# Kernel optimization log

Measured on AMD Instinct MI355X. Metric: run time of the kernel, lower is better.

## Reference

```python
import jax, jax.numpy as jnp
import numpy as np

B, T, N, D, K, H = 32, 24, 2048, 64, 32, 16  # batch, timesteps, nodes, dim_in=dim_out, embed_dim, HT_Tem


def setup_inputs() -> dict:
    key = jax.random.key(0)
    ks = jax.random.split(key, 6)
    return {
        "eb": jax.random.normal(ks[0], (B, T, N, D), dtype=jnp.float32),
        "node_embeddings": jax.random.normal(ks[1], (N, K), dtype=jnp.float32),
        "time_eb": jax.random.normal(ks[2], (B, T, K), dtype=jnp.float32),
        "adj": jax.random.normal(ks[3], (K, H, T), dtype=jnp.float32),
        "weights_pool": jax.random.normal(ks[4], (K, D, D), dtype=jnp.float32),
        "bias_pool": jax.random.normal(ks[5], (K, D), dtype=jnp.float32),
    }


def reference(eb, node_embeddings, time_eb, adj, weights_pool, bias_pool):
    # adj_dynamics: [H, T, N] (torch computes nht then permutes to htn)
    adj_dyn = jnp.einsum('nk,kht->htn', node_embeddings, adj)
    # hypergraph aggregation: [B, H, N, D]
    hyper = jnp.einsum('htn,btnd->bhnd', adj_dyn, eb)
    # de-aggregation back to time axis: [B, T, N, D]
    ret = jnp.einsum('htn,bhnd->btnd', adj_dyn, hyper)
    # per-(b,t) generated weights [B, T, D, D] and bias [B, T, 1, D]
    weights = jnp.einsum('btd,dio->btio', time_eb, weights_pool)
    bias = jnp.einsum('btd,do->bto', time_eb, bias_pool)[:, :, None, :]
    out = jnp.einsum('btni,btio->btno', ret, weights) + bias
    return jax.nn.leaky_relu(out + eb, negative_slope=0.01)
```

## Files before the change

### kernel.cpp

```cpp
#include <hip/hip_runtime.h>

#define B_ 32
#define T_ 24
#define N_ 2048
#define D_ 64
#define K_ 32
#define H_ 16
#define NB 16

typedef __attribute__((ext_vector_type(8))) short bf16x8;
typedef __attribute__((ext_vector_type(4))) float f32x4;

__device__ __forceinline__ unsigned short f2bf(float f) {
    unsigned int u = __float_as_uint(f);
    return (unsigned short)((u + 0x7FFFu + ((u >> 16) & 1u)) >> 16);
}
__device__ __forceinline__ float bf2f(unsigned short h) {
    return __uint_as_float(((unsigned int)h) << 16);
}

__global__ void k_prepM(const float* __restrict__ ne, const float* __restrict__ adj,
                        unsigned short* __restrict__ M2) {
    __shared__ float s_ne[K_];
    __shared__ float s_ad[H_ * T_];
    const int n = blockIdx.x;
    const int tid = threadIdx.x;
    if (tid < K_) s_ne[tid] = ne[n * K_ + tid];
    __syncthreads();
    for (int f = tid; f < H_ * T_; f += 64) {
        const int h = f / T_, t = f % T_;
        float a = 0.f;
#pragma unroll
        for (int k = 0; k < K_; ++k) a += s_ne[k] * adj[(k * H_ + h) * T_ + t];
        s_ad[f] = a;
    }
    __syncthreads();
    unsigned short* dst = M2 + (size_t)(n >> 4) * (T_ * T_ * 16) + (n & 15) * T_;
    for (int m = tid; m < T_ * T_; m += 64) {
        const int t = m / T_, t2 = m % T_;
        float a = 0.f;
#pragma unroll
        for (int h = 0; h < H_; ++h) a += s_ad[h * T_ + t] * s_ad[h * T_ + t2];
        dst[t * (16 * T_) + t2] = f2bf(a);
    }
}

__global__ __launch_bounds__(256) void k_prepW(const float* __restrict__ te,
                                               const float* __restrict__ wp,
                                               const float* __restrict__ bp,
                                               unsigned short* __restrict__ Wt,
                                               float* __restrict__ bias) {
    const int bt = blockIdx.x;
    const int tid = threadIdx.x;
    __shared__ float s_te[K_];
    __shared__ float s_W[D_ * D_];
    if (tid < K_) s_te[tid] = te[bt * K_ + tid];
    __syncthreads();
    float4 acc[4] = {};
    for (int k = 0; k < K_; ++k) {
        const float tk = s_te[k];
        const float4* row = (const float4*)(wp + (size_t)k * (D_ * D_));
#pragma unroll
        for (int i = 0; i < 4; ++i) {
            float4 v = row[tid + i * 256];
            acc[i].x += tk * v.x; acc[i].y += tk * v.y;
            acc[i].z += tk * v.z; acc[i].w += tk * v.w;
        }
    }
    float4* sW4 = (float4*)s_W;
#pragma unroll
    for (int i = 0; i < 4; ++i) sW4[tid + i * 256] = acc[i];
    if (tid < D_) {
        float a = 0.f;
#pragma unroll
        for (int k = 0; k < K_; ++k) a += s_te[k] * bp[k * D_ + tid];
        bias[bt * D_ + tid] = a;
    }
    __syncthreads();
    const int o = tid >> 2;
    const int i0 = (tid & 3) * 16;
    unsigned short* dst = Wt + (size_t)bt * (D_ * D_) + o * D_ + i0;
#pragma unroll
    for (int j = 0; j < 16; j += 4) {
        ushort4 u;
        u.x = f2bf(s_W[(i0 + j + 0) * D_ + o]);
        u.y = f2bf(s_W[(i0 + j + 1) * D_ + o]);
        u.z = f2bf(s_W[(i0 + j + 2) * D_ + o]);
        u.w = f2bf(s_W[(i0 + j + 3) * D_ + o]);
        *(ushort4*)(dst + j) = u;
    }
}

__global__ __launch_bounds__(512, 2) void k_fused(const float* __restrict__ eb,
                                                  const unsigned short* __restrict__ M2,
                                                  const unsigned short* __restrict__ Wt,
                                                  const float* __restrict__ bias,
                                                  float* __restrict__ out) {
    const int b = blockIdx.y;
    const int nb = blockIdx.x * NB;
    const int tid = threadIdx.x;
    const int wave = tid >> 6, lane = tid & 63;
    const int lr = lane & 15, lh = lane >> 4;

    __shared__ unsigned short s_eb[T_ * NB * D_];
    __shared__ unsigned short s_M[T_ * NB * T_];

    {
        const float* ebb = eb + (size_t)(b * T_) * N_ * D_;
#pragma unroll
        for (int it = 0; it < 12; ++it) {
            const int f4 = it * 512 + tid;
            const int t = f4 >> 8;
            const int n = (f4 >> 4) & 15;
            const int d0 = (f4 & 15) * 4;
            const float4 v = *(const float4*)(ebb + ((size_t)t * N_ + nb + n) * D_ + d0);
            ushort4 u;
            u.x = f2bf(v.x); u.y = f2bf(v.y); u.z = f2bf(v.z); u.w = f2bf(v.w);
            const int inrow = (d0 * 2) ^ ((n & 7) << 4);
            *(ushort4*)((char*)s_eb + t * (NB * 128) + n * 128 + inrow) = u;
        }
    }
    {
        const unsigned short* Mblk = M2 + (size_t)blockIdx.x * (T_ * T_ * 16);
#pragma unroll
        for (int it = 0; it < 18; ++it) {
            const int e = it * 512 + tid;
            s_M[e] = Mblk[e];
        }
    }
    __syncthreads();

    const char* ebase = (const char*)s_eb;
    const int sw = (lr & 7) << 4;
    const int tb = wave * 3;

    const unsigned short* mrow = s_M + tb * (16 * T_) + lr * T_;
    const char* base0 = ebase + lr * 128 + ((lh * 16) ^ sw);
    const char* base1 = ebase + lr * 128 + ((((lh + 4) * 16)) ^ sw);

    float acc[3][16];
#pragma unroll
    for (int tt = 0; tt < 3; ++tt)
#pragma unroll
        for (int j = 0; j < 16; ++j) acc[tt][j] = 0.f;

#pragma unroll
    for (int tp = 0; tp < T_; ++tp) {
        const float m0 = bf2f(mrow[tp]);
        const float m1 = bf2f(mrow[384 + tp]);
        const float m2 = bf2f(mrow[768 + tp]);
        const bf16x8 e0 = *(const bf16x8*)(base0 + tp * 2048);
        const bf16x8 e1 = *(const bf16x8*)(base1 + tp * 2048);
#pragma unroll
        for (int q = 0; q < 8; ++q) {
            const float ea = bf2f((unsigned short)e0[q]);
            const float eb2 = bf2f((unsigned short)e1[q]);
            acc[0][q] += m0 * ea; acc[0][8 + q] += m0 * eb2;
            acc[1][q] += m1 * ea; acc[1][8 + q] += m1 * eb2;
            acc[2][q] += m2 * ea; acc[2][8 + q] += m2 * eb2;
        }
    }

    bf16x8 Af[3][2];
#pragma unroll
    for (int tt = 0; tt < 3; ++tt)
#pragma unroll
        for (int j = 0; j < 8; ++j) {
            Af[tt][0][j] = (short)f2bf(acc[tt][j]);
            Af[tt][1][j] = (short)f2bf(acc[tt][8 + j]);
        }

#pragma unroll
    for (int tt = 0; tt < 3; ++tt) {
        const int t = tb + tt;
        const int bt = b * T_ + t;
        const unsigned short* Wb = Wt + (size_t)bt * (D_ * D_);
        f32x4 C[4] = {};
#pragma unroll
        for (int ot = 0; ot < 4; ++ot) {
            const bf16x8 B0 = *(const bf16x8*)(Wb + (ot * 16 + lr) * D_ + lh * 8);
            const bf16x8 B1 = *(const bf16x8*)(Wb + (ot * 16 + lr) * D_ + 32 + lh * 8);
            C[ot] = __builtin_amdgcn_mfma_f32_16x16x32_bf16(Af[tt][0], B0, C[ot], 0, 0, 0);
            C[ot] = __builtin_amdgcn_mfma_f32_16x16x32_bf16(Af[tt][1], B1, C[ot], 0, 0, 0);
        }
        float bv[4];
#pragma unroll
        for (int ot = 0; ot < 4; ++ot) bv[ot] = bias[bt * D_ + ot * 16 + lr];

        float* obt = out + ((size_t)bt * N_ + nb) * D_;
#pragma unroll
        for (int r = 0; r < 4; ++r) {
            const int nn = lh * 4 + r;
            const char* erow = ebase + (t * NB + nn) * 128;
            const int swn = (nn & 7) << 4;
#pragma unroll
            for (int ot = 0; ot < 4; ++ot) {
                const int o = ot * 16 + lr;
                const unsigned short eu =
                    *(const unsigned short*)(erow + ((o * 2) ^ swn));
                float v = C[ot][r] + bv[ot] + bf2f(eu);
                v = v >= 0.f ? v : 0.01f * v;
                obt[(size_t)nn * D_ + o] = v;
            }
        }
    }
}

extern "C" void kernel_launch(void* const* d_in, const int* in_sizes, int n_in,
                              void* d_out, int out_size, void* d_ws, size_t ws_size,
                              hipStream_t stream) {
    const float* eb  = (const float*)d_in[0];
    const float* ne  = (const float*)d_in[1];
    const float* te  = (const float*)d_in[2];
    const float* adj = (const float*)d_in[3];
    const float* wp  = (const float*)d_in[4];
    const float* bp  = (const float*)d_in[5];
    float* out = (float*)d_out;

    char* ws = (char*)d_ws;
    const size_t M_bytes  = (size_t)N_ * T_ * T_ * 2;
    const size_t Wt_bytes = (size_t)B_ * T_ * D_ * D_ * 2;
    unsigned short* M2 = (unsigned short*)ws;
    unsigned short* Wt = (unsigned short*)(ws + M_bytes);
    float* bias        = (float*)(ws + M_bytes + Wt_bytes);

    k_prepM<<<N_, 64, 0, stream>>>(ne, adj, M2);
    k_prepW<<<B_ * T_, 256, 0, stream>>>(te, wp, bp, Wt, bias);
    k_fused<<<dim3(N_ / NB, B_), 512, 0, stream>>>(eb, M2, Wt, bias, out);
}
```

Baseline: 284.6 us.

## Shrink node tile to 8, remap lanes, build MFMA A-fragments via ds_bpermute

Halves the node block to 8 with 256-thread blocks, each wave running two passes over timesteps. Each lane now accumulates 8 d-values for one node, and the MFMA A operand is assembled from those lanes with ds_bpermute. The bias and residual are preloaded into the MFMA accumulator, and the shared-memory swizzle is redone for the new layout. The aim is a smaller LDS footprint and more resident blocks; the cost is half-empty MFMA rows (only 8 of 16 used), duplicated W loads per block, and extra permute instructions.

```diff
diff --git a/kernel.cpp b/kernel.cpp
--- a/kernel.cpp
+++ b/kernel.cpp
@@ -6,10 +6,11 @@
 #define D_ 64
 #define K_ 32
 #define H_ 16
-#define NB 16
+#define NB 8
 
 typedef __attribute__((ext_vector_type(8))) short bf16x8;
 typedef __attribute__((ext_vector_type(4))) float f32x4;
+typedef __attribute__((ext_vector_type(4))) int i32x4;
 
 __device__ __forceinline__ unsigned short f2bf(float f) {
     unsigned int u = __float_as_uint(f);
@@ -35,13 +36,13 @@
         s_ad[f] = a;
     }
     __syncthreads();
-    unsigned short* dst = M2 + (size_t)(n >> 4) * (T_ * T_ * 16) + (n & 15) * T_;
+    unsigned short* dst = M2 + (size_t)(n >> 3) * (T_ * T_ * NB) + (n & 7) * T_;
     for (int m = tid; m < T_ * T_; m += 64) {
         const int t = m / T_, t2 = m % T_;
         float a = 0.f;
 #pragma unroll
         for (int h = 0; h < H_; ++h) a += s_ad[h * T_ + t] * s_ad[h * T_ + t2];
-        dst[t * (16 * T_) + t2] = f2bf(a);
+        dst[t * (NB * T_) + t2] = f2bf(a);
     }
 }
 
@@ -91,7 +92,7 @@
     }
 }
 
-__global__ __launch_bounds__(512, 2) void k_fused(const float* __restrict__ eb,
+__global__ __launch_bounds__(256, 4) void k_fused(const float* __restrict__ eb,
                                                   const unsigned short* __restrict__ M2,
                                                   const unsigned short* __restrict__ Wt,
                                                   const float* __restrict__ bias,
@@ -101,106 +102,123 @@
     const int tid = threadIdx.x;
     const int wave = tid >> 6, lane = tid & 63;
     const int lr = lane & 15, lh = lane >> 4;
+    const int ln = lane & 7;
+    const int dh = lane >> 3;
 
     __shared__ unsigned short s_eb[T_ * NB * D_];
     __shared__ unsigned short s_M[T_ * NB * T_];
 
     {
-        const float* ebb = eb + (size_t)(b * T_) * N_ * D_;
 #pragma unroll
         for (int it = 0; it < 12; ++it) {
-            const int f4 = it * 512 + tid;
-            const int t = f4 >> 8;
-            const int n = (f4 >> 4) & 15;
-            const int d0 = (f4 & 15) * 4;
-            const float4 v = *(const float4*)(ebb + ((size_t)t * N_ + nb + n) * D_ + d0);
+            const int f4 = it * 256 + tid;
+            const int t = f4 >> 7;
+            const int rem = f4 & 127;
+            const int n = rem >> 4;
+            const int d0 = (rem & 15) * 4;
+            const float4 v = *(const float4*)(eb + ((size_t)(b * T_ + t) * N_ + nb + n) * D_ + d0);
             ushort4 u;
             u.x = f2bf(v.x); u.y = f2bf(v.y); u.z = f2bf(v.z); u.w = f2bf(v.w);
-            const int inrow = (d0 * 2) ^ ((n & 7) << 4);
-            *(ushort4*)((char*)s_eb + t * (NB * 128) + n * 128 + inrow) = u;
+            const int dh0 = d0 >> 3;
+            const int slot = dh0 * 8 + (n ^ dh0);
+            *(ushort4*)((char*)s_eb + t * 1024 + slot * 16 + (d0 & 7) * 2) = u;
         }
     }
     {
-        const unsigned short* Mblk = M2 + (size_t)blockIdx.x * (T_ * T_ * 16);
-#pragma unroll
-        for (int it = 0; it < 18; ++it) {
-            const int e = it * 512 + tid;
-            s_M[e] = Mblk[e];
-        }
-    }
-    __syncthreads();
-
-    const char* ebase = (const char*)s_eb;
-    const int sw = (lr & 7) << 4;
-    const int tb = wave * 3;
-
-    const unsigned short* mrow = s_M + tb * (16 * T_) + lr * T_;
-    const char* base0 = ebase + lr * 128 + ((lh * 16) ^ sw);
-    const char* base1 = ebase + lr * 128 + ((((lh + 4) * 16)) ^ sw);
-
-    float acc[3][16];
-#pragma unroll
-    for (int tt = 0; tt < 3; ++tt)
-#pragma unroll
-        for (int j = 0; j < 16; ++j) acc[tt][j] = 0.f;
-
-#pragma unroll
-    for (int tp = 0; tp < T_; ++tp) {
-        const float m0 = bf2f(mrow[tp]);
-        const float m1 = bf2f(mrow[384 + tp]);
-        const float m2 = bf2f(mrow[768 + tp]);
-        const bf16x8 e0 = *(const bf16x8*)(base0 + tp * 2048);
-        const bf16x8 e1 = *(const bf16x8*)(base1 + tp * 2048);
-#pragma unroll
-        for (int q = 0; q < 8; ++q) {
-            const float ea = bf2f((unsigned short)e0[q]);
-            const float eb2 = bf2f((unsigned short)e1[q]);
-            acc[0][q] += m0 * ea; acc[0][8 + q] += m0 * eb2;
-            acc[1][q] += m1 * ea; acc[1][8 + q] += m1 * eb2;
-            acc[2][q] += m2 * ea; acc[2][8 + q] += m2 * eb2;
-        }
-    }
-
-    bf16x8 Af[3][2];
-#pragma unroll
-    for (int tt = 0; tt < 3; ++tt)
-#pragma unroll
-        for (int j = 0; j < 8; ++j) {
-            Af[tt][0][j] = (short)f2bf(acc[tt][j]);
-            Af[tt][1][j] = (short)f2bf(acc[tt][8 + j]);
-        }
-
-#pragma unroll
-    for (int tt = 0; tt < 3; ++tt) {
-        const int t = tb + tt;
-        const int bt = b * T_ + t;
-        const unsigned short* Wb = Wt + (size_t)bt * (D_ * D_);
-        f32x4 C[4] = {};
-#pragma unroll
-        for (int ot = 0; ot < 4; ++ot) {
-            const bf16x8 B0 = *(const bf16x8*)(Wb + (ot * 16 + lr) * D_ + lh * 8);
-            const bf16x8 B1 = *(const bf16x8*)(Wb + (ot * 16 + lr) * D_ + 32 + lh * 8);
-            C[ot] = __builtin_amdgcn_mfma_f32_16x16x32_bf16(Af[tt][0], B0, C[ot], 0, 0, 0);
-            C[ot] = __builtin_amdgcn_mfma_f32_16x16x32_bf16(Af[tt][1], B1, C[ot], 0, 0, 0);
-        }
-        float bv[4];
-#pragma unroll
-        for (int ot = 0; ot < 4; ++ot) bv[ot] = bias[bt * D_ + ot * 16 + lr];
-
-        float* obt = out + ((size_t)bt * N_ + nb) * D_;
-#pragma unroll
-        for (int r = 0; r < 4; ++r) {
-            const int nn = lh * 4 + r;
-            const char* erow = ebase + (t * NB + nn) * 128;
-            const int swn = (nn & 7) << 4;
+        const unsigned int* Mg = (const unsigned int*)(M2 + (size_t)blockIdx.x * (T_ * T_ * NB));
+        unsigned int* Ml = (unsigned int*)s_M;
+#pragma unroll
+        for (int i = 0; i < 9; ++i) Ml[i * 256 + tid] = Mg[i * 256 + tid];
+    }
+    __syncthreads();
+
+    const char* ebase = (const char*)s_eb + (dh * 8 + (ln ^ dh)) * 16;
+    const unsigned short* mrow = s_M + ln * T_;
+    const int addr0 = (lh * 8 + ln) * 4;
+    const int addr1 = ((lh + 4) * 8 + ln) * 4;
+
+    for (int pass = 0; pass < 2; ++pass) {
+        const int tb = pass * 12 + wave * 3;
+
+        float acc[3][8];
+#pragma unroll
+        for (int tt = 0; tt < 3; ++tt)
+#pragma unroll
+            for (int q = 0; q < 8; ++q) acc[tt][q] = 0.f;
+
+#pragma unroll 4
+        for (int tp = 0; tp < T_; ++tp) {
+            const float m0 = bf2f(mrow[(tb + 0) * 192 + tp]);
+            const float m1 = bf2f(mrow[(tb + 1) * 192 + tp]);
+            const float m2 = bf2f(mrow[(tb + 2) * 192 + tp]);
+            const bf16x8 e = *(const bf16x8*)(ebase + tp * 1024);
+#pragma unroll
+            for (int q = 0; q < 8; ++q) {
+                const float ef = bf2f((unsigned short)e[q]);
+                acc[0][q] += m0 * ef;
+                acc[1][q] += m1 * ef;
+                acc[2][q] += m2 * ef;
+            }
+        }
+
+#pragma unroll
+        for (int tt = 0; tt < 3; ++tt) {
+            const int t = tb + tt;
+            const int bt = b * T_ + t;
+
+            const int w0 = (int)((unsigned)f2bf(acc[tt][0]) | ((unsigned)f2bf(acc[tt][1]) << 16));
+            const int w1 = (int)((unsigned)f2bf(acc[tt][2]) | ((unsigned)f2bf(acc[tt][3]) << 16));
+            const int w2 = (int)((unsigned)f2bf(acc[tt][4]) | ((unsigned)f2bf(acc[tt][5]) << 16));
+            const int w3 = (int)((unsigned)f2bf(acc[tt][6]) | ((unsigned)f2bf(acc[tt][7]) << 16));
+
+            i32x4 a0v, a1v;
+            a0v.x = __builtin_amdgcn_ds_bpermute(addr0, w0);
+            a0v.y = __builtin_amdgcn_ds_bpermute(addr0, w1);
+            a0v.z = __builtin_amdgcn_ds_bpermute(addr0, w2);
+            a0v.w = __builtin_amdgcn_ds_bpermute(addr0, w3);
+            a1v.x = __builtin_amdgcn_ds_bpermute(addr1, w0);
+            a1v.y = __builtin_amdgcn_ds_bpermute(addr1, w1);
+            a1v.z = __builtin_amdgcn_ds_bpermute(addr1, w2);
+            a1v.w = __builtin_amdgcn_ds_bpermute(addr1, w3);
+            const bf16x8 Af0 = __builtin_bit_cast(bf16x8, a0v);
+            const bf16x8 Af1 = __builtin_bit_cast(bf16x8, a1v);
+
+            const unsigned short* Wb = Wt + (size_t)bt * (D_ * D_);
+            f32x4 C[4];
 #pragma unroll
             for (int ot = 0; ot < 4; ++ot) {
                 const int o = ot * 16 + lr;
-                const unsigned short eu =
-                    *(const unsigned short*)(erow + ((o * 2) ^ swn));
-                float v = C[ot][r] + bv[ot] + bf2f(eu);
-                v = v >= 0.f ? v : 0.01f * v;
-                obt[(size_t)nn * D_ + o] = v;
+                const float bv = bias[bt * D_ + o];
+                const int dho = o >> 3;
+#pragma unroll
+                for (int r = 0; r < 4; ++r) {
+                    const int nn = (lh & 1) * 4 + r;
+                    const unsigned short ev = *(const unsigned short*)(
+                        (const char*)s_eb + t * 1024 + (dho * 8 + (nn ^ dho)) * 16 + (o & 7) * 2);
+                    C[ot][r] = bv + bf2f(ev);
+                }
+            }
+#pragma unroll
+            for (int ot = 0; ot < 4; ++ot) {
+                const bf16x8 B0 = *(const bf16x8*)(Wb + (ot * 16 + lr) * D_ + lh * 8);
+                const bf16x8 B1 = *(const bf16x8*)(Wb + (ot * 16 + lr) * D_ + 32 + lh * 8);
+                C[ot] = __builtin_amdgcn_mfma_f32_16x16x32_bf16(Af0, B0, C[ot], 0, 0, 0);
+                C[ot] = __builtin_amdgcn_mfma_f32_16x16x32_bf16(Af1, B1, C[ot], 0, 0, 0);
+            }
+
+            if (lh < 2) {
+                float* obt = out + ((size_t)bt * N_ + nb) * D_;
+#pragma unroll
+                for (int ot = 0; ot < 4; ++ot) {
+                    const int o = ot * 16 + lr;
+#pragma unroll
+                    for (int r = 0; r < 4; ++r) {
+                        const int nn = lh * 4 + r;
+                        float v = C[ot][r];
+                        v = v >= 0.f ? v : 0.01f * v;
+                        obt[(size_t)nn * D_ + o] = v;
+                    }
+                }
             }
         }
     }
@@ -226,5 +244,5 @@
 
     k_prepM<<<N_, 64, 0, stream>>>(ne, adj, M2);
     k_prepW<<<B_ * T_, 256, 0, stream>>>(te, wp, bp, Wt, bias);
-    k_fused<<<dim3(N_ / NB, B_), 512, 0, stream>>>(eb, M2, Wt, bias, out);
-}
+    k_fused<<<dim3(N_ / NB, B_), 256, 0, stream>>>(eb, M2, Wt, bias, out);
+}
```

Result: slower. 317.1 us (+11.4%).
